# Optimization experiments

Measured on AMD Instinct MI355X. Metric: run time of the kernel, lower is better.

Reference implementation:

```python
import jax, jax.numpy as jnp
import numpy as np

H = 16          # nhead
EPS = 1e-5      # LayerNorm eps (torch default)


def _layernorm(x, g, b):
    mu = jnp.mean(x, axis=-1, keepdims=True)
    var = jnp.mean(jnp.square(x - mu), axis=-1, keepdims=True)
    return (x - mu) * jax.lax.rsqrt(var + EPS) * g + b


def setup_inputs() -> dict:
    key = jax.random.key(0)
    ks = jax.random.split(key, 8)
    B, L, D, F = 256, 64, 1024, 4096
    s = 0.02
    return {
        "src": jax.random.normal(ks[0], (B, L, D), jnp.float32),
        "Wq": jax.random.normal(ks[1], (D, D), jnp.float32) * s,
        "bq": jnp.zeros((D,), jnp.float32),
        "Wk": jax.random.normal(ks[2], (D, D), jnp.float32) * s,
        "bk": jnp.zeros((D,), jnp.float32),
        "Wv": jax.random.normal(ks[3], (D, D), jnp.float32) * s,
        "bv": jnp.zeros((D,), jnp.float32),
        "Wo": jax.random.normal(ks[4], (D, D), jnp.float32) * s,
        "bo": jnp.zeros((D,), jnp.float32),
        "rel_bias": jax.random.normal(ks[5], (H, 2 * L - 1), jnp.float32) * s,
        "W1": jax.random.normal(ks[6], (D, F), jnp.float32) * s,
        "b1": jnp.zeros((F,), jnp.float32),
        "W2": jax.random.normal(ks[7], (F, D), jnp.float32) * s,
        "b2": jnp.zeros((D,), jnp.float32),
        "g1": jnp.ones((D,), jnp.float32),
        "be1": jnp.zeros((D,), jnp.float32),
        "g2": jnp.ones((D,), jnp.float32),
        "be2": jnp.zeros((D,), jnp.float32),
    }


def reference(src, Wq, bq, Wk, bk, Wv, bv, Wo, bo, rel_bias,
              W1, b1, W2, b2, g1, be1, g2, be2):
    B, L, D = src.shape
    dh = D // H
    # --- relative multi-head attention ---
    q = (src @ Wq + bq).reshape(B, L, H, dh)
    k = (src @ Wk + bk).reshape(B, L, H, dh)
    v = (src @ Wv + bv).reshape(B, L, H, dh)
    scores = jnp.einsum('bqhd,bkhd->bhqk', q, k) / jnp.sqrt(jnp.float32(dh))
    # relative position bias lookup: index i - j + (L-1) into (H, 2L-1) table
    rel_idx = jnp.arange(L)[:, None] - jnp.arange(L)[None, :] + (L - 1)  # (L,L)
    scores = scores + rel_bias[:, rel_idx]  # broadcast (H,L,L) over batch
    attn = jax.nn.softmax(scores, axis=-1)
    ctx = jnp.einsum('bhqk,bkhd->bqhd', attn, v).reshape(B, L, D)
    attn_out = ctx @ Wo + bo
    # --- residual + LN + FFN + residual + LN (dropout = eval no-op) ---
    x = _layernorm(src + attn_out, g1, be1)
    ff = jax.nn.gelu(x @ W1 + b1) @ W2 + b2
    return _layernorm(x + ff, g2, be2)
```

## Files before the change

kernel.cpp:

```cpp
#include <hip/hip_runtime.h>

typedef __bf16 bf16;
typedef __attribute__((ext_vector_type(8))) __bf16 bf16x8;
typedef __attribute__((ext_vector_type(4))) __bf16 bf16x4;
typedef __attribute__((ext_vector_type(4))) float f32x4;

#define N_TOK 16384
#define DMODEL 1024
#define FDIM 4096
#define NHEAD 16

__device__ __forceinline__ void gload_lds16(const bf16* g, bf16* l) {
  __builtin_amdgcn_global_load_lds(
      (const __attribute__((address_space(1))) void*)g,
      (__attribute__((address_space(3))) void*)l,
      16, 0, 0);
}

__device__ __forceinline__ float gelu_tanh(float x) {
  return 0.5f * x * (1.0f + tanhf(0.7978845608028654f * (x + 0.044715f * x * x * x)));
}

__global__ __launch_bounds__(256) void cvt_copy(const float* __restrict__ x,
                                                bf16* __restrict__ y) {
  size_t i = ((size_t)blockIdx.x * 256 + threadIdx.x) * 8;
  float4 a = *(const float4*)(x + i);
  float4 b = *(const float4*)(x + i + 4);
  bf16x8 o;
  o[0] = (bf16)a.x; o[1] = (bf16)a.y; o[2] = (bf16)a.z; o[3] = (bf16)a.w;
  o[4] = (bf16)b.x; o[5] = (bf16)b.y; o[6] = (bf16)b.z; o[7] = (bf16)b.w;
  *(bf16x8*)(y + i) = o;
}

__global__ void convt(const float* __restrict__ src, bf16* __restrict__ dst,
                      int R, int C) {
  __shared__ float tile[32][33];
  int c0 = blockIdx.x * 32, r0 = blockIdx.y * 32;
  int tx = threadIdx.x, ty = threadIdx.y;
#pragma unroll
  for (int i = 0; i < 4; ++i)
    tile[ty * 4 + i][tx] = src[(size_t)(r0 + ty * 4 + i) * C + c0 + tx];
  __syncthreads();
#pragma unroll
  for (int i = 0; i < 4; ++i)
    dst[(size_t)(c0 + ty * 4 + i) * R + r0 + tx] = (bf16)tile[tx][ty * 4 + i];
}


__device__ __forceinline__ void stage_half(const bf16* g, int ldg, bf16* region,
                                           int wv, int lane) {
#pragma unroll
  for (int j = 0; j < 2; ++j) {
    int c = wv * 2 + j;
    int r = c * 8 + (lane >> 3);
    int col = ((lane & 7) * 8) ^ ((r & 7) * 8);
    gload_lds16(g + (size_t)r * ldg + col, region + c * 512 + lane * 8);
  }
}

__device__ __forceinline__ bf16x8 frag_ld(const bf16* s, int row, int kc) {
  return *(const bf16x8*)(s + row * 64 + (kc ^ ((row & 7) * 8)));
}

template <int RES, int GELU>
__global__ __launch_bounds__(512) void gemm256(
    const bf16* __restrict__ A, const bf16* __restrict__ BT,
    const float* __restrict__ bias, const float* __restrict__ resf,
    const bf16* __restrict__ resb, bf16* __restrict__ C,
    int M, int N, int K) {
  __shared__ alignas(16) bf16 sA[2][256 * 64];
  __shared__ alignas(16) bf16 sB[2][256 * 64];
  const int tid = threadIdx.x;
  const int lane = tid & 63, wv = tid >> 6;
  const int wr = wv >> 2, wc = wv & 3;
  const int r16 = lane & 15, hk = lane >> 4;

  const int nbn = N >> 8;
  const int cpx = gridDim.x >> 3;
  const int swz = ((int)blockIdx.x & 7) * cpx + ((int)blockIdx.x >> 3);
  const int row0 = (swz / nbn) << 8, col0 = (swz % nbn) << 8;

  const bf16* Ab = A + (size_t)row0 * K;
  const bf16* Bb = BT + (size_t)col0 * K;

  f32x4 acc[8][4] = {};
  bf16x8 aF[4][2], bF0[2][2], bF1[2][2];

  stage_half(Ab,                      K, &sA[0][0],        wv, lane);
  stage_half(Ab + 128 * (size_t)K,    K, &sA[0][128 * 64], wv, lane);
  stage_half(Bb,                      K, &sB[0][0],        wv, lane);
  stage_half(Bb + 128 * (size_t)K,    K, &sB[0][128 * 64], wv, lane);
  asm volatile("s_waitcnt vmcnt(0)" ::: "memory");
  __builtin_amdgcn_s_barrier();

  const int nt = K >> 6;
  for (int kt = 0; kt < nt; ++kt) {
    const bf16* sa = &sA[kt & 1][0];
    const bf16* sb = &sB[kt & 1][0];
    bf16* na = &sA[(kt + 1) & 1][0];
    bf16* nb = &sB[(kt + 1) & 1][0];
    const bool pf = (kt + 1 < nt);
    const size_t koff = (size_t)(kt + 1) << 6;

#pragma unroll
    for (int i = 0; i < 4; ++i)
#pragma unroll
      for (int ks = 0; ks < 2; ++ks)
        aF[i][ks] = frag_ld(sa, wr * 128 + i * 16 + r16, ks * 32 + hk * 8);
#pragma unroll
    for (int j = 0; j < 2; ++j)
#pragma unroll
      for (int ks = 0; ks < 2; ++ks)
        bF0[j][ks] = frag_ld(sb, wc * 64 + j * 16 + r16, ks * 32 + hk * 8);
    if (pf) {
      stage_half(Ab + koff,                   K, na,            wv, lane);
      stage_half(Ab + 128 * (size_t)K + koff, K, na + 128 * 64, wv, lane);
    }
    __builtin_amdgcn_s_barrier();
    __builtin_amdgcn_s_setprio(1);
#pragma unroll
    for (int i = 0; i < 4; ++i)
#pragma unroll
      for (int j = 0; j < 2; ++j)
#pragma unroll
        for (int ks = 0; ks < 2; ++ks)
          acc[i][j] = __builtin_amdgcn_mfma_f32_16x16x32_bf16(bF0[j][ks], aF[i][ks], acc[i][j], 0, 0, 0);
    __builtin_amdgcn_s_setprio(0);
    __builtin_amdgcn_s_barrier();

#pragma unroll
    for (int j = 0; j < 2; ++j)
#pragma unroll
      for (int ks = 0; ks < 2; ++ks)
        bF1[j][ks] = frag_ld(sb, wc * 64 + (2 + j) * 16 + r16, ks * 32 + hk * 8);
    if (pf) {
      stage_half(Bb + koff,                   K, nb,            wv, lane);
      stage_half(Bb + 128 * (size_t)K + koff, K, nb + 128 * 64, wv, lane);
    }
    __builtin_amdgcn_s_barrier();
    __builtin_amdgcn_s_setprio(1);
#pragma unroll
    for (int i = 0; i < 4; ++i)
#pragma unroll
      for (int j = 0; j < 2; ++j)
#pragma unroll
        for (int ks = 0; ks < 2; ++ks)
          acc[i][2 + j] = __builtin_amdgcn_mfma_f32_16x16x32_bf16(bF1[j][ks], aF[i][ks], acc[i][2 + j], 0, 0, 0);
    __builtin_amdgcn_s_setprio(0);
    __builtin_amdgcn_s_barrier();

#pragma unroll
    for (int i = 0; i < 4; ++i)
#pragma unroll
      for (int ks = 0; ks < 2; ++ks)
        aF[i][ks] = frag_ld(sa, wr * 128 + (4 + i) * 16 + r16, ks * 32 + hk * 8);
    __builtin_amdgcn_s_barrier();
    __builtin_amdgcn_s_setprio(1);
#pragma unroll
    for (int i = 0; i < 4; ++i)
#pragma unroll
      for (int j = 0; j < 2; ++j)
#pragma unroll
        for (int ks = 0; ks < 2; ++ks)
          acc[4 + i][2 + j] = __builtin_amdgcn_mfma_f32_16x16x32_bf16(bF1[j][ks], aF[i][ks], acc[4 + i][2 + j], 0, 0, 0);
    __builtin_amdgcn_s_setprio(0);
    __builtin_amdgcn_s_barrier();

    __builtin_amdgcn_s_setprio(1);
#pragma unroll
    for (int i = 0; i < 4; ++i)
#pragma unroll
      for (int j = 0; j < 2; ++j)
#pragma unroll
        for (int ks = 0; ks < 2; ++ks)
          acc[4 + i][j] = __builtin_amdgcn_mfma_f32_16x16x32_bf16(bF0[j][ks], aF[i][ks], acc[4 + i][j], 0, 0, 0);
    __builtin_amdgcn_s_setprio(0);
    asm volatile("s_waitcnt vmcnt(0)" ::: "memory");
    __builtin_amdgcn_s_barrier();
  }

#pragma unroll
  for (int m = 0; m < 8; ++m) {
    int row = row0 + wr * 128 + m * 16 + r16;
#pragma unroll
    for (int n = 0; n < 4; ++n) {
      int col = col0 + wc * 64 + n * 16 + hk * 4;
      f32x4 b4 = *(const f32x4*)&bias[col];
      f32x4 v;
#pragma unroll
      for (int r = 0; r < 4; ++r) v[r] = acc[m][n][r] + b4[r];
      if (RES == 1) {
        f32x4 rr = *(const f32x4*)&resf[(size_t)row * N + col];
#pragma unroll
        for (int r = 0; r < 4; ++r) v[r] += rr[r];
      }
      if (RES == 2) {
        bf16x4 rb = *(const bf16x4*)&resb[(size_t)row * N + col];
#pragma unroll
        for (int r = 0; r < 4; ++r) v[r] += (float)rb[r];
      }
      bf16x4 o;
#pragma unroll
      for (int r = 0; r < 4; ++r) {
        float x = v[r];
        if (GELU) x = gelu_tanh(x);
        o[r] = (bf16)x;
      }
      *(bf16x4*)&C[(size_t)row * N + col] = o;
    }
  }
}

__global__ __launch_bounds__(256) void attn_k(
    const bf16* q, const bf16* __restrict__ k,
    const bf16* __restrict__ v, const float* __restrict__ rel,
    bf16* ctx) {
  __shared__ alignas(16) bf16 lQ[64 * 64];
  __shared__ alignas(16) bf16 lK[64 * 64];
  __shared__ alignas(16) bf16 lVt[64 * 64];
  __shared__ alignas(16) bf16 lP[4][16 * 64];
  __shared__ float lrel[128];

  const int bh = blockIdx.x;
  const int b = bh >> 4, h = bh & 15;
  const int tid = threadIdx.x;
  const size_t base = (size_t)(b * 64) * DMODEL + h * 64;

#pragma unroll
  for (int i = 0; i < 2; ++i) {
    int j = (tid >> 3) + i * 32;
    int d0 = (tid & 7) * 8;
    *(bf16x8*)&lQ[j * 64 + d0] = *(const bf16x8*)(q + base + (size_t)j * DMODEL + d0);
    *(bf16x8*)&lK[j * 64 + d0] = *(const bf16x8*)(k + base + (size_t)j * DMODEL + d0);
    bf16x8 vvv = *(const bf16x8*)(v + base + (size_t)j * DMODEL + d0);
#pragma unroll
    for (int u = 0; u < 8; ++u) lVt[(d0 + u) * 64 + j] = vvv[u];
  }
  if (tid < 127) lrel[tid] = rel[h * 127 + tid];
  __syncthreads();

  const int lane = tid & 63, w = tid >> 6;
  const int r16 = lane & 15, hk = lane >> 4;

  f32x4 s[4] = {};
#pragma unroll
  for (int dstep = 0; dstep < 2; ++dstep) {
    bf16x8 aq = *(const bf16x8*)&lQ[(w * 16 + r16) * 64 + dstep * 32 + hk * 8];
#pragma unroll
    for (int n = 0; n < 4; ++n) {
      bf16x8 bk_ = *(const bf16x8*)&lK[(n * 16 + r16) * 64 + dstep * 32 + hk * 8];
      s[n] = __builtin_amdgcn_mfma_f32_16x16x32_bf16(aq, bk_, s[n], 0, 0, 0);
    }
  }

  float p[16];
#pragma unroll
  for (int n = 0; n < 4; ++n)
#pragma unroll
    for (int r = 0; r < 4; ++r) {
      int i = w * 16 + hk * 4 + r;
      int j = n * 16 + r16;
      p[n * 4 + r] = s[n][r] * 0.125f + lrel[i - j + 63];
    }
#pragma unroll
  for (int r = 0; r < 4; ++r) {
    float m = fmaxf(fmaxf(p[r], p[4 + r]), fmaxf(p[8 + r], p[12 + r]));
#pragma unroll
    for (int off = 1; off < 16; off <<= 1) m = fmaxf(m, __shfl_xor(m, off));
    float sum = 0.f;
#pragma unroll
    for (int n = 0; n < 4; ++n) {
      p[n * 4 + r] = __expf(p[n * 4 + r] - m);
      sum += p[n * 4 + r];
    }
#pragma unroll
    for (int off = 1; off < 16; off <<= 1) sum += __shfl_xor(sum, off);
    float inv = 1.0f / sum;
#pragma unroll
    for (int n = 0; n < 4; ++n) p[n * 4 + r] *= inv;
  }
#pragma unroll
  for (int n = 0; n < 4; ++n)
#pragma unroll
    for (int r = 0; r < 4; ++r)
      lP[w][(hk * 4 + r) * 64 + n * 16 + r16] = (bf16)p[n * 4 + r];
  __syncthreads();

  f32x4 o[4] = {};
#pragma unroll
  for (int ks = 0; ks < 2; ++ks) {
    bf16x8 ap = *(const bf16x8*)&lP[w][r16 * 64 + ks * 32 + hk * 8];
#pragma unroll
    for (int n = 0; n < 4; ++n) {
      bf16x8 bv_ = *(const bf16x8*)&lVt[(n * 16 + r16) * 64 + ks * 32 + hk * 8];
      o[n] = __builtin_amdgcn_mfma_f32_16x16x32_bf16(ap, bv_, o[n], 0, 0, 0);
    }
  }
#pragma unroll
  for (int n = 0; n < 4; ++n)
#pragma unroll
    for (int r = 0; r < 4; ++r) {
      int trow = b * 64 + w * 16 + hk * 4 + r;
      ctx[(size_t)trow * DMODEL + h * 64 + n * 16 + r16] = (bf16)o[n][r];
    }
}

template <int F32OUT>
__global__ __launch_bounds__(256) void layernorm_k(
    const bf16* __restrict__ x, const float* __restrict__ g,
    const float* __restrict__ be, bf16* __restrict__ ob,
    float* __restrict__ of) {
  int row = blockIdx.x * 4 + (threadIdx.x >> 6);
  int lane = threadIdx.x & 63;
  const bf16* xr = x + (size_t)row * DMODEL + lane * 16;
  bf16x8 v0 = *(const bf16x8*)xr;
  bf16x8 v1 = *(const bf16x8*)(xr + 8);
  float f[16];
#pragma unroll
  for (int j = 0; j < 8; ++j) { f[j] = (float)v0[j]; f[8 + j] = (float)v1[j]; }
  float s = 0.f, sq = 0.f;
#pragma unroll
  for (int j = 0; j < 16; ++j) { s += f[j]; sq += f[j] * f[j]; }
#pragma unroll
  for (int off = 1; off < 64; off <<= 1) {
    s += __shfl_xor(s, off);
    sq += __shfl_xor(sq, off);
  }
  float mean = s * (1.0f / DMODEL);
  float var = sq * (1.0f / DMODEL) - mean * mean;
  float rstd = rsqrtf(var + 1e-5f);
  const float* gp = g + lane * 16;
  const float* bp = be + lane * 16;
  if (F32OUT) {
    float* op = of + (size_t)row * DMODEL + lane * 16;
#pragma unroll
    for (int j = 0; j < 16; ++j)
      op[j] = (f[j] - mean) * rstd * gp[j] + bp[j];
  } else {
    bf16x8 o0, o1;
#pragma unroll
    for (int j = 0; j < 8; ++j) {
      o0[j] = (bf16)((f[j] - mean) * rstd * gp[j] + bp[j]);
      o1[j] = (bf16)((f[8 + j] - mean) * rstd * gp[8 + j] + bp[8 + j]);
    }
    bf16* op = ob + (size_t)row * DMODEL + lane * 16;
    *(bf16x8*)op = o0;
    *(bf16x8*)(op + 8) = o1;
  }
}

extern "C" void kernel_launch(void* const* d_in, const int* in_sizes, int n_in,
                              void* d_out, int out_size, void* d_ws, size_t ws_size,
                              hipStream_t stream) {
  (void)in_sizes; (void)n_in; (void)out_size; (void)ws_size;
  const float* src = (const float*)d_in[0];
  const float* Wq  = (const float*)d_in[1];
  const float* bq  = (const float*)d_in[2];
  const float* Wk  = (const float*)d_in[3];
  const float* bk  = (const float*)d_in[4];
  const float* Wv  = (const float*)d_in[5];
  const float* bv  = (const float*)d_in[6];
  const float* Wo  = (const float*)d_in[7];
  const float* bo  = (const float*)d_in[8];
  const float* rel = (const float*)d_in[9];
  const float* W1  = (const float*)d_in[10];
  const float* b1  = (const float*)d_in[11];
  const float* W2  = (const float*)d_in[12];
  const float* b2  = (const float*)d_in[13];
  const float* g1  = (const float*)d_in[14];
  const float* be1 = (const float*)d_in[15];
  const float* g2  = (const float*)d_in[16];
  const float* be2 = (const float*)d_in[17];

  char* ws = (char*)d_ws;
  const size_t MiB = 1ull << 20;
  bf16* srcb = (bf16*)(ws + 0 * MiB);
  bf16* qb   = (bf16*)(ws + 32 * MiB);
  bf16* WqT  = (bf16*)(ws + 64 * MiB);
  bf16* WkT  = (bf16*)(ws + 66 * MiB);
  bf16* WvT  = (bf16*)(ws + 68 * MiB);
  bf16* WoT  = (bf16*)(ws + 70 * MiB);
  bf16* W1T  = (bf16*)(ws + 72 * MiB);
  bf16* W2T  = (bf16*)(ws + 80 * MiB);
  bf16* hbuf = (bf16*)(ws + 0 * MiB);
  float* lnout = (float*)(ws + 0 * MiB);
  bf16* kb = (bf16*)d_out;
  bf16* vb = (bf16*)((char*)d_out + 32 * MiB);
  bf16* y1 = kb;
  bf16* xb = vb;
  bf16* y2 = kb;

  cvt_copy<<<(N_TOK * DMODEL) / 2048, 256, 0, stream>>>(src, srcb);
  dim3 tb(32, 8);
  convt<<<dim3(32, 32), tb, 0, stream>>>(Wq, WqT, 1024, 1024);
  convt<<<dim3(32, 32), tb, 0, stream>>>(Wk, WkT, 1024, 1024);
  convt<<<dim3(32, 32), tb, 0, stream>>>(Wv, WvT, 1024, 1024);
  convt<<<dim3(32, 32), tb, 0, stream>>>(Wo, WoT, 1024, 1024);
  convt<<<dim3(128, 32), tb, 0, stream>>>(W1, W1T, 1024, 4096);
  convt<<<dim3(32, 128), tb, 0, stream>>>(W2, W2T, 4096, 1024);

  const int gQKV = (N_TOK / 256) * (DMODEL / 256);
  gemm256<0, 0><<<gQKV, 512, 0, stream>>>(srcb, WqT, bq, nullptr, nullptr, qb, N_TOK, DMODEL, DMODEL);
  gemm256<0, 0><<<gQKV, 512, 0, stream>>>(srcb, WkT, bk, nullptr, nullptr, kb, N_TOK, DMODEL, DMODEL);
  gemm256<0, 0><<<gQKV, 512, 0, stream>>>(srcb, WvT, bv, nullptr, nullptr, vb, N_TOK, DMODEL, DMODEL);

  attn_k<<<256 * NHEAD, 256, 0, stream>>>(qb, kb, vb, rel, qb);

  gemm256<1, 0><<<gQKV, 512, 0, stream>>>(qb, WoT, bo, src, nullptr, y1, N_TOK, DMODEL, DMODEL);
  layernorm_k<0><<<N_TOK / 4, 256, 0, stream>>>(y1, g1, be1, xb, nullptr);

  const int CH = 8192;
  const int gF1 = (CH / 256) * (FDIM / 256);
  const int gF2 = (CH / 256) * (DMODEL / 256);
  for (int c = 0; c < 2; ++c) {
    const bf16* xc = xb + (size_t)c * CH * DMODEL;
    bf16* yc = y2 + (size_t)c * CH * DMODEL;
    gemm256<0, 1><<<gF1, 512, 0, stream>>>(xc, W1T, b1, nullptr, nullptr, hbuf, CH, FDIM, DMODEL);
    gemm256<2, 0><<<gF2, 512, 0, stream>>>(hbuf, W2T, b2, nullptr, xc, yc, CH, DMODEL, FDIM);
  }
  layernorm_k<1><<<N_TOK / 4, 256, 0, stream>>>(y2, g2, be2, nullptr, lnout);
  hipMemcpyAsync(d_out, lnout, (size_t)N_TOK * DMODEL * 4, hipMemcpyDeviceToDevice, stream);
}
```

Measured before the change: 723.9 us.

## Deepen GEMM prefetch pipeline, use 128-row tiles for FFN2, skip final memcpy

The GEMM is rewritten to prefetch two k-tiles ahead into the buffer just consumed, using partial vmcnt waits instead of draining all loads every iteration. A BM template parameter lets the FFN down-projection use 128-row tiles, doubling its grid to improve CU occupancy. When the workspace is large enough, y2 goes to a separate workspace region so the final layernorm writes straight into the output and the 64 MiB device-to-device copy is dropped. Risks include getting the vmcnt counts wrong and the reuse of the current buffer being unsafe if the barriers do not cover it.

Result: faster. 633.3 us (-12.5%).

```diff
diff --git a/kernel.cpp b/kernel.cpp
--- a/kernel.cpp
+++ b/kernel.cpp
@@ -46,30 +46,18 @@
     dst[(size_t)(c0 + ty * 4 + i) * R + r0 + tx] = (bf16)tile[tx][ty * 4 + i];
 }
 
-
-__device__ __forceinline__ void stage_half(const bf16* g, int ldg, bf16* region,
-                                           int wv, int lane) {
-#pragma unroll
-  for (int j = 0; j < 2; ++j) {
-    int c = wv * 2 + j;
-    int r = c * 8 + (lane >> 3);
-    int col = ((lane & 7) * 8) ^ ((r & 7) * 8);
-    gload_lds16(g + (size_t)r * ldg + col, region + c * 512 + lane * 8);
-  }
-}
-
-__device__ __forceinline__ bf16x8 frag_ld(const bf16* s, int row, int kc) {
-  return *(const bf16x8*)(s + row * 64 + (kc ^ ((row & 7) * 8)));
-}
-
-template <int RES, int GELU>
-__global__ __launch_bounds__(512) void gemm256(
+template <int BM_, int RES, int GELU>
+__global__ __launch_bounds__(512) void gemm_c(
     const bf16* __restrict__ A, const bf16* __restrict__ BT,
     const float* __restrict__ bias, const float* __restrict__ resf,
     const bf16* __restrict__ resb, bf16* __restrict__ C,
     int M, int N, int K) {
-  __shared__ alignas(16) bf16 sA[2][256 * 64];
+  constexpr int ALOADS = BM_ / 64;
+  constexpr int MH = BM_ / 32;
+  constexpr int MQ = MH / 2;
+  __shared__ alignas(16) bf16 sA[2][BM_ * 64];
   __shared__ alignas(16) bf16 sB[2][256 * 64];
+
   const int tid = threadIdx.x;
   const int lane = tid & 63, wv = tid >> 6;
   const int wr = wv >> 2, wc = wv & 3;
@@ -78,110 +66,128 @@
   const int nbn = N >> 8;
   const int cpx = gridDim.x >> 3;
   const int swz = ((int)blockIdx.x & 7) * cpx + ((int)blockIdx.x >> 3);
-  const int row0 = (swz / nbn) << 8, col0 = (swz % nbn) << 8;
+  const int row0 = (swz / nbn) * BM_, col0 = (swz % nbn) << 8;
 
   const bf16* Ab = A + (size_t)row0 * K;
   const bf16* Bb = BT + (size_t)col0 * K;
 
-  f32x4 acc[8][4] = {};
-  bf16x8 aF[4][2], bF0[2][2], bF1[2][2];
-
-  stage_half(Ab,                      K, &sA[0][0],        wv, lane);
-  stage_half(Ab + 128 * (size_t)K,    K, &sA[0][128 * 64], wv, lane);
-  stage_half(Bb,                      K, &sB[0][0],        wv, lane);
-  stage_half(Bb + 128 * (size_t)K,    K, &sB[0][128 * 64], wv, lane);
-  asm volatile("s_waitcnt vmcnt(0)" ::: "memory");
+  auto stageA = [&](int buf, int kt) {
+#pragma unroll
+    for (int l = 0; l < ALOADS; ++l) {
+      int g = l * 512 + tid;
+      int r = g >> 3, p = g & 7;
+      gload_lds16(Ab + (size_t)r * K + ((size_t)kt << 6) + ((p ^ (r & 7)) << 3),
+                  &sA[buf][g * 8]);
+    }
+  };
+  auto stageB = [&](int buf, int kt) {
+#pragma unroll
+    for (int l = 0; l < 4; ++l) {
+      int g = l * 512 + tid;
+      int r = g >> 3, p = g & 7;
+      gload_lds16(Bb + (size_t)r * K + ((size_t)kt << 6) + ((p ^ (r & 7)) << 3),
+                  &sB[buf][g * 8]);
+    }
+  };
+  auto frag = [&](const bf16* s, int row, int kc) -> bf16x8 {
+    return *(const bf16x8*)(s + row * 64 + (kc ^ ((row & 7) * 8)));
+  };
+
+  f32x4 acc[MH][4] = {};
+  bf16x8 aF[MQ][2], bF0[2][2], bF1[2][2];
+
+  const int nt = K >> 6;
+  stageA(0, 0); stageB(0, 0);
+  stageA(1, 1); stageB(1, 1);
+  if constexpr (BM_ == 256) asm volatile("s_waitcnt vmcnt(8)" ::: "memory");
+  else                      asm volatile("s_waitcnt vmcnt(6)" ::: "memory");
   __builtin_amdgcn_s_barrier();
 
-  const int nt = K >> 6;
   for (int kt = 0; kt < nt; ++kt) {
-    const bf16* sa = &sA[kt & 1][0];
-    const bf16* sb = &sB[kt & 1][0];
-    bf16* na = &sA[(kt + 1) & 1][0];
-    bf16* nb = &sB[(kt + 1) & 1][0];
-    const bool pf = (kt + 1 < nt);
-    const size_t koff = (size_t)(kt + 1) << 6;
-
-#pragma unroll
-    for (int i = 0; i < 4; ++i)
+    const int cb = kt & 1;
+    const bf16* sa = &sA[cb][0];
+    const bf16* sb = &sB[cb][0];
+    const bool pf = (kt + 2 < nt);
+
+#pragma unroll
+    for (int m = 0; m < MQ; ++m)
 #pragma unroll
       for (int ks = 0; ks < 2; ++ks)
-        aF[i][ks] = frag_ld(sa, wr * 128 + i * 16 + r16, ks * 32 + hk * 8);
-#pragma unroll
-    for (int j = 0; j < 2; ++j)
+        aF[m][ks] = frag(sa, wr * (BM_ / 2) + m * 16 + r16, ks * 32 + hk * 8);
+#pragma unroll
+    for (int n = 0; n < 2; ++n)
 #pragma unroll
       for (int ks = 0; ks < 2; ++ks)
-        bF0[j][ks] = frag_ld(sb, wc * 64 + j * 16 + r16, ks * 32 + hk * 8);
+        bF0[n][ks] = frag(sb, wc * 64 + n * 16 + r16, ks * 32 + hk * 8);
+    __builtin_amdgcn_s_barrier();
+    __builtin_amdgcn_s_setprio(1);
+#pragma unroll
+    for (int m = 0; m < MQ; ++m)
+#pragma unroll
+      for (int n = 0; n < 2; ++n)
+#pragma unroll
+        for (int ks = 0; ks < 2; ++ks)
+          acc[m][n] = __builtin_amdgcn_mfma_f32_16x16x32_bf16(bF0[n][ks], aF[m][ks], acc[m][n], 0, 0, 0);
+    __builtin_amdgcn_s_setprio(0);
+    __builtin_amdgcn_s_barrier();
+
+#pragma unroll
+    for (int n = 0; n < 2; ++n)
+#pragma unroll
+      for (int ks = 0; ks < 2; ++ks)
+        bF1[n][ks] = frag(sb, wc * 64 + (2 + n) * 16 + r16, ks * 32 + hk * 8);
+    __builtin_amdgcn_s_barrier();
+    __builtin_amdgcn_s_setprio(1);
+#pragma unroll
+    for (int m = 0; m < MQ; ++m)
+#pragma unroll
+      for (int n = 0; n < 2; ++n)
+#pragma unroll
+        for (int ks = 0; ks < 2; ++ks)
+          acc[m][2 + n] = __builtin_amdgcn_mfma_f32_16x16x32_bf16(bF1[n][ks], aF[m][ks], acc[m][2 + n], 0, 0, 0);
+    __builtin_amdgcn_s_setprio(0);
+    __builtin_amdgcn_s_barrier();
+
+#pragma unroll
+    for (int m = 0; m < MQ; ++m)
+#pragma unroll
+      for (int ks = 0; ks < 2; ++ks)
+        aF[m][ks] = frag(sa, wr * (BM_ / 2) + (MQ + m) * 16 + r16, ks * 32 + hk * 8);
+    if (pf) stageB(cb, kt + 2);
+    __builtin_amdgcn_s_barrier();
+    __builtin_amdgcn_s_setprio(1);
+#pragma unroll
+    for (int m = 0; m < MQ; ++m)
+#pragma unroll
+      for (int n = 0; n < 2; ++n)
+#pragma unroll
+        for (int ks = 0; ks < 2; ++ks)
+          acc[MQ + m][2 + n] = __builtin_amdgcn_mfma_f32_16x16x32_bf16(bF1[n][ks], aF[m][ks], acc[MQ + m][2 + n], 0, 0, 0);
+    __builtin_amdgcn_s_setprio(0);
+    __builtin_amdgcn_s_barrier();
+
+    if (pf) stageA(cb, kt + 2);
+    __builtin_amdgcn_s_setprio(1);
+#pragma unroll
+    for (int m = 0; m < MQ; ++m)
+#pragma unroll
+      for (int n = 0; n < 2; ++n)
+#pragma unroll
+        for (int ks = 0; ks < 2; ++ks)
+          acc[MQ + m][n] = __builtin_amdgcn_mfma_f32_16x16x32_bf16(bF0[n][ks], aF[m][ks], acc[MQ + m][n], 0, 0, 0);
+    __builtin_amdgcn_s_setprio(0);
     if (pf) {
-      stage_half(Ab + koff,                   K, na,            wv, lane);
-      stage_half(Ab + 128 * (size_t)K + koff, K, na + 128 * 64, wv, lane);
-    }
-    __builtin_amdgcn_s_barrier();
-    __builtin_amdgcn_s_setprio(1);
-#pragma unroll
-    for (int i = 0; i < 4; ++i)
-#pragma unroll
-      for (int j = 0; j < 2; ++j)
-#pragma unroll
-        for (int ks = 0; ks < 2; ++ks)
-          acc[i][j] = __builtin_amdgcn_mfma_f32_16x16x32_bf16(bF0[j][ks], aF[i][ks], acc[i][j], 0, 0, 0);
-    __builtin_amdgcn_s_setprio(0);
-    __builtin_amdgcn_s_barrier();
-
-#pragma unroll
-    for (int j = 0; j < 2; ++j)
-#pragma unroll
-      for (int ks = 0; ks < 2; ++ks)
-        bF1[j][ks] = frag_ld(sb, wc * 64 + (2 + j) * 16 + r16, ks * 32 + hk * 8);
-    if (pf) {
-      stage_half(Bb + koff,                   K, nb,            wv, lane);
-      stage_half(Bb + 128 * (size_t)K + koff, K, nb + 128 * 64, wv, lane);
-    }
-    __builtin_amdgcn_s_barrier();
-    __builtin_amdgcn_s_setprio(1);
-#pragma unroll
-    for (int i = 0; i < 4; ++i)
-#pragma unroll
-      for (int j = 0; j < 2; ++j)
-#pragma unroll
-        for (int ks = 0; ks < 2; ++ks)
-          acc[i][2 + j] = __builtin_amdgcn_mfma_f32_16x16x32_bf16(bF1[j][ks], aF[i][ks], acc[i][2 + j], 0, 0, 0);
-    __builtin_amdgcn_s_setprio(0);
-    __builtin_amdgcn_s_barrier();
-
-#pragma unroll
-    for (int i = 0; i < 4; ++i)
-#pragma unroll
-      for (int ks = 0; ks < 2; ++ks)
-        aF[i][ks] = frag_ld(sa, wr * 128 + (4 + i) * 16 + r16, ks * 32 + hk * 8);
-    __builtin_amdgcn_s_barrier();
-    __builtin_amdgcn_s_setprio(1);
-#pragma unroll
-    for (int i = 0; i < 4; ++i)
-#pragma unroll
-      for (int j = 0; j < 2; ++j)
-#pragma unroll
-        for (int ks = 0; ks < 2; ++ks)
-          acc[4 + i][2 + j] = __builtin_amdgcn_mfma_f32_16x16x32_bf16(bF1[j][ks], aF[i][ks], acc[4 + i][2 + j], 0, 0, 0);
-    __builtin_amdgcn_s_setprio(0);
-    __builtin_amdgcn_s_barrier();
-
-    __builtin_amdgcn_s_setprio(1);
-#pragma unroll
-    for (int i = 0; i < 4; ++i)
-#pragma unroll
-      for (int j = 0; j < 2; ++j)
-#pragma unroll
-        for (int ks = 0; ks < 2; ++ks)
-          acc[4 + i][j] = __builtin_amdgcn_mfma_f32_16x16x32_bf16(bF0[j][ks], aF[i][ks], acc[4 + i][j], 0, 0, 0);
-    __builtin_amdgcn_s_setprio(0);
-    asm volatile("s_waitcnt vmcnt(0)" ::: "memory");
-    __builtin_amdgcn_s_barrier();
-  }
-
-#pragma unroll
-  for (int m = 0; m < 8; ++m) {
-    int row = row0 + wr * 128 + m * 16 + r16;
+      if constexpr (BM_ == 256) asm volatile("s_waitcnt vmcnt(8)" ::: "memory");
+      else                      asm volatile("s_waitcnt vmcnt(6)" ::: "memory");
+    } else if (kt + 1 < nt) {
+      asm volatile("s_waitcnt vmcnt(0)" ::: "memory");
+    }
+    __builtin_amdgcn_s_barrier();
+  }
+
+#pragma unroll
+  for (int m = 0; m < MH; ++m) {
+    int row = row0 + wr * (BM_ / 2) + m * 16 + r16;
 #pragma unroll
     for (int n = 0; n < 4; ++n) {
       int col = col0 + wc * 64 + n * 16 + hk * 4;
@@ -352,7 +358,7 @@
 extern "C" void kernel_launch(void* const* d_in, const int* in_sizes, int n_in,
                               void* d_out, int out_size, void* d_ws, size_t ws_size,
                               hipStream_t stream) {
-  (void)in_sizes; (void)n_in; (void)out_size; (void)ws_size;
+  (void)in_sizes; (void)n_in; (void)out_size;
   const float* src = (const float*)d_in[0];
   const float* Wq  = (const float*)d_in[1];
   const float* bq  = (const float*)d_in[2];
@@ -388,7 +394,8 @@
   bf16* vb = (bf16*)((char*)d_out + 32 * MiB);
   bf16* y1 = kb;
   bf16* xb = vb;
-  bf16* y2 = kb;
+  const bool bigws = (ws_size >= 121 * MiB);
+  bf16* y2 = bigws ? (bf16*)(ws + 88 * MiB) : kb;
 
   cvt_copy<<<(N_TOK * DMODEL) / 2048, 256, 0, stream>>>(src, srcb);
   dim3 tb(32, 8);
@@ -400,24 +407,28 @@
   convt<<<dim3(32, 128), tb, 0, stream>>>(W2, W2T, 4096, 1024);
 
   const int gQKV = (N_TOK / 256) * (DMODEL / 256);
-  gemm256<0, 0><<<gQKV, 512, 0, stream>>>(srcb, WqT, bq, nullptr, nullptr, qb, N_TOK, DMODEL, DMODEL);
-  gemm256<0, 0><<<gQKV, 512, 0, stream>>>(srcb, WkT, bk, nullptr, nullptr, kb, N_TOK, DMODEL, DMODEL);
-  gemm256<0, 0><<<gQKV, 512, 0, stream>>>(srcb, WvT, bv, nullptr, nullptr, vb, N_TOK, DMODEL, DMODEL);
+  gemm_c<256, 0, 0><<<gQKV, 512, 0, stream>>>(srcb, WqT, bq, nullptr, nullptr, qb, N_TOK, DMODEL, DMODEL);
+  gemm_c<256, 0, 0><<<gQKV, 512, 0, stream>>>(srcb, WkT, bk, nullptr, nullptr, kb, N_TOK, DMODEL, DMODEL);
+  gemm_c<256, 0, 0><<<gQKV, 512, 0, stream>>>(srcb, WvT, bv, nullptr, nullptr, vb, N_TOK, DMODEL, DMODEL);
 
   attn_k<<<256 * NHEAD, 256, 0, stream>>>(qb, kb, vb, rel, qb);
 
-  gemm256<1, 0><<<gQKV, 512, 0, stream>>>(qb, WoT, bo, src, nullptr, y1, N_TOK, DMODEL, DMODEL);
+  gemm_c<256, 1, 0><<<gQKV, 512, 0, stream>>>(qb, WoT, bo, src, nullptr, y1, N_TOK, DMODEL, DMODEL);
   layernorm_k<0><<<N_TOK / 4, 256, 0, stream>>>(y1, g1, be1, xb, nullptr);
 
   const int CH = 8192;
   const int gF1 = (CH / 256) * (FDIM / 256);
-  const int gF2 = (CH / 256) * (DMODEL / 256);
+  const int gF2 = (CH / 128) * (DMODEL / 256);
   for (int c = 0; c < 2; ++c) {
     const bf16* xc = xb + (size_t)c * CH * DMODEL;
     bf16* yc = y2 + (size_t)c * CH * DMODEL;
-    gemm256<0, 1><<<gF1, 512, 0, stream>>>(xc, W1T, b1, nullptr, nullptr, hbuf, CH, FDIM, DMODEL);
-    gemm256<2, 0><<<gF2, 512, 0, stream>>>(hbuf, W2T, b2, nullptr, xc, yc, CH, DMODEL, FDIM);
-  }
-  layernorm_k<1><<<N_TOK / 4, 256, 0, stream>>>(y2, g2, be2, nullptr, lnout);
-  hipMemcpyAsync(d_out, lnout, (size_t)N_TOK * DMODEL * 4, hipMemcpyDeviceToDevice, stream);
-}
+    gemm_c<256, 0, 1><<<gF1, 512, 0, stream>>>(xc, W1T, b1, nullptr, nullptr, hbuf, CH, FDIM, DMODEL);
+    gemm_c<128, 2, 0><<<gF2, 512, 0, stream>>>(hbuf, W2T, b2, nullptr, xc, yc, CH, DMODEL, FDIM);
+  }
+  if (bigws) {
+    layernorm_k<1><<<N_TOK / 4, 256, 0, stream>>>(y2, g2, be2, nullptr, (float*)d_out);
+  } else {
+    layernorm_k<1><<<N_TOK / 4, 256, 0, stream>>>(y2, g2, be2, nullptr, lnout);
+    hipMemcpyAsync(d_out, lnout, (size_t)N_TOK * DMODEL * 4, hipMemcpyDeviceToDevice, stream);
+  }
+}
```
